# Kernel optimization log

Measured on AMD Instinct MI355X. Metric: run time of the kernel, lower is better.

The kernel has to match this reference:

```python
import math
import jax, jax.numpy as jnp
import numpy as np

INPUT_DIM = 1024
HEADS = 16
SEQ = 4096
BATCH = 1
SCALE = math.sqrt(INPUT_DIM / HEADS)  # 8.0


def setup_inputs() -> dict:
    key = jax.random.key(0)
    ks = jax.random.split(key, 5)
    D = INPUT_DIM
    return {
        "x": jax.random.normal(ks[0], (BATCH, SEQ, D), dtype=jnp.float32),
        "w_qkv": jax.random.normal(ks[1], (3 * D, D), dtype=jnp.float32) * (1.0 / math.sqrt(D)),
        "b_qkv": jax.random.normal(ks[2], (3 * D,), dtype=jnp.float32) * 0.01,
        "w_out": jax.random.normal(ks[3], (D, D), dtype=jnp.float32) * (1.0 / math.sqrt(D)),
        "b_out": jax.random.normal(ks[4], (D,), dtype=jnp.float32) * 0.01,
    }


def reference(x, w_qkv, b_qkv, w_out, b_out):
    b, n, D = x.shape
    h = HEADS
    d = D // h
    # qkv projection: [b, n, 3D]
    qkv = x @ w_qkv.T + b_qkv
    # 'b n (c h d) -> b c h n d' with c=3 outermost
    qkv = qkv.reshape(b, n, 3, h, d).transpose(2, 0, 3, 1, 4)  # [3, b, h, n, d]
    q, k, v = qkv[0], qkv[1], qkv[2]
    q = q / SCALE
    attn = jnp.einsum('bhnd,bhmd->bhnm', q, k)  # [b, h, n, n]
    attn = jax.nn.softmax(attn, axis=-1)
    # dropout is identity in eval mode
    context = jnp.einsum('bhnm,bhmd->bhnd', attn, v)  # [b, h, n, d]
    context = context.transpose(0, 2, 1, 3).reshape(b, n, D)  # 'b h n d -> b n (h d)'
    return context @ w_out.T + b_out
```

## Files before the change

### kernel.cpp

```cpp
#include <hip/hip_runtime.h>

typedef unsigned short u16;
typedef unsigned int u32;
typedef __attribute__((ext_vector_type(8))) short short8;
typedef __attribute__((ext_vector_type(4))) float f32x4;

__device__ __forceinline__ u16 f2b(float f) {
  union { float f; unsigned u; } v; v.f = f;
  unsigned r = (v.u + 0x7FFFu + ((v.u >> 16) & 1u)) >> 16;
  return (u16)r;
}
__device__ __forceinline__ float b2f(u16 b) {
  union { unsigned u; float f; } v; v.u = ((unsigned)b) << 16;
  return v.f;
}
__device__ __forceinline__ u32 cvtpk(float a, float b) {
  u32 r;
  asm("v_cvt_pk_bf16_f32 %0, %1, %2" : "=v"(r) : "v"(a), "v"(b));
  return r;
}
__device__ __forceinline__ void p32swap(u32& a, u32& b) {
  asm("v_permlane32_swap_b32 %0, %1" : "+v"(a), "+v"(b));
}
__device__ __forceinline__ void p16swap(u32& a, u32& b) {
  asm("v_permlane16_swap_b32 %0, %1" : "+v"(a), "+v"(b));
}
__device__ __forceinline__ float ldf(const void* p, size_t i, int f32) {
  return f32 ? ((const float*)p)[i] : b2f(((const u16*)p)[i]);
}

__global__ __launch_bounds__(256) void detect_dtype(const u16* __restrict__ x,
                                                    int* __restrict__ flag) {
  __shared__ int cnt;
  if (threadIdx.x == 0) cnt = 0;
  __syncthreads();
  int local = 0;
  for (int p = threadIdx.x; p < 512; p += 256) {
    int e = (x[2 * p] >> 7) & 0xFF;
    if (e >= 0xC0) local++;
  }
  atomicAdd(&cnt, local);
  __syncthreads();
  if (threadIdx.x == 0) flag[0] = (cnt >= 16) ? 1 : 0;
}

__global__ __launch_bounds__(256) void convert_all(
    const void* __restrict__ px, const void* __restrict__ pwq,
    const void* __restrict__ pbq, const void* __restrict__ pwo,
    const void* __restrict__ pbo, u16* __restrict__ xb,
    u16* __restrict__ wqkvb, u16* __restrict__ bqkvb, u16* __restrict__ wob,
    u16* __restrict__ bob) {
  __shared__ int sf;
  if (threadIdx.x == 0) sf = 0;
  __syncthreads();
  {
    const u16* xr = (const u16*)px;
    int local = 0;
    for (int p = threadIdx.x; p < 512; p += 256) {
      int e = (xr[2 * p] >> 7) & 0xFF;
      if (e >= 0xC0) local++;
    }
    atomicAdd(&sf, local);
  }
  __syncthreads();
  const int isf32 = (sf >= 16);

  int i = blockIdx.x * 256 + threadIdx.x;
  const void* in; u16* out; size_t g;
  if (i < 524288)       { in = px;  out = xb;    g = (size_t)i; }
  else if (i < 917504)  { in = pwq; out = wqkvb; g = (size_t)(i - 524288); }
  else if (i < 917888)  { in = pbq; out = bqkvb; g = (size_t)(i - 917504); }
  else if (i < 1048960) { in = pwo; out = wob;   g = (size_t)(i - 917888); }
  else                  { in = pbo; out = bob;   g = (size_t)(i - 1048960); }
  size_t base = g * 8;
  if (isf32) {
    const float* p = (const float*)in + base;
    float4 v0 = *(const float4*)p, v1 = *(const float4*)(p + 4);
    union { short8 v; u16 e[8]; } t;
    t.e[0]=f2b(v0.x); t.e[1]=f2b(v0.y); t.e[2]=f2b(v0.z); t.e[3]=f2b(v0.w);
    t.e[4]=f2b(v1.x); t.e[5]=f2b(v1.y); t.e[6]=f2b(v1.z); t.e[7]=f2b(v1.w);
    *(short8*)(out + base) = t.v;
  } else {
    *(short8*)(out + base) = *(const short8*)((const u16*)in + base);
  }
}

__global__ __launch_bounds__(256) void transpose_v(const u16* __restrict__ qkv,
                                                   u16* __restrict__ Vt) {
  __shared__ u16 T[64 * 72];
  const int tid = threadIdx.x;
  const int h = blockIdx.y;
  const int s0 = blockIdx.x * 64;
  for (int r = 0; r < 2; ++r) {
    int cid = r * 256 + tid;
    int s = cid >> 3, c8 = cid & 7;
    union { short8 v; u16 u[8]; } uu;
    uu.v = *(const short8*)(qkv + (size_t)(s0 + s) * 3072 + 2048 + h * 64 + c8 * 8);
    for (int i = 0; i < 8; ++i) T[(c8 * 8 + i) * 72 + s] = uu.u[i];
  }
  __syncthreads();
  for (int r = 0; r < 2; ++r) {
    int cid = r * 256 + tid;
    int dd = cid >> 3, c8 = cid & 7;
    union { short8 v; u16 u[8]; } uu;
    for (int i = 0; i < 8; ++i) uu.u[i] = T[dd * 72 + c8 * 8 + i];
    *(short8*)(Vt + (size_t)(h * 64 + dd) * 4096 + s0 + c8 * 8) = uu.v;
  }
}

__global__ __launch_bounds__(256) void gemm_bt(const void* __restrict__ A,
                                               const void* __restrict__ B,
                                               const void* __restrict__ bias,
                                               void* __restrict__ C,
                                               int M, int N, int K,
                                               int lda, int ldb, int ldc,
                                               int aMay, int bMay, int outF32,
                                               const int* __restrict__ flag) {
  __shared__ __align__(16) u16 sm[128 * 132];
  u16* As = sm;
  u16* Bs = sm + 128 * 64;
  const int f = flag[0];
  const int a32 = aMay && f, b32 = bMay && f;
  const int tid = threadIdx.x;
  const int w = tid >> 6, lane = tid & 63;
  const int lq = lane & 15, qr = lane >> 4;
  const int m0 = blockIdx.y * 128, n0 = blockIdx.x * 128;
  const int wm = (w >> 1) * 64, wn = (w & 1) * 64;

  f32x4 acc[4][4];
  for (int i = 0; i < 4; i++)
    for (int j = 0; j < 4; j++) acc[i][j] = (f32x4){0.f, 0.f, 0.f, 0.f};
  float bv[4];
  for (int ns = 0; ns < 4; ++ns) bv[ns] = ldf(bias, n0 + wn + ns * 16 + lq, b32);

  const int rs = tid >> 3, cs = tid & 7;
  const u16* gA = (const u16*)A + (size_t)(m0 + rs) * lda + cs * 8;
  const u16* gB = (const u16*)B + (size_t)(n0 + rs) * ldb + cs * 8;
  u16* lA = As + ((tid & ~63) << 3);
  u16* lB = Bs + ((tid & ~63) << 3);

  for (int k0 = 0; k0 < K; k0 += 64) {
    if (!(a32 | b32)) {
      for (int r = 0; r < 4; ++r) {
        __builtin_amdgcn_global_load_lds(gA + (size_t)(r * 32) * lda + k0,
                                         lA + r * 2048, 16, 0, 0);
        __builtin_amdgcn_global_load_lds(gB + (size_t)(r * 32) * ldb + k0,
                                         lB + r * 2048, 16, 0, 0);
      }
    } else {
      for (int r = 0; r < 4; ++r) {
        int cid = r * 256 + tid;
        int row = cid >> 3, c = cid & 7;
        if (a32) {
          const float* p = (const float*)A + (size_t)(m0 + row) * lda + k0 + c * 8;
          float4 v0 = *(const float4*)p, v1 = *(const float4*)(p + 4);
          union { short8 v; u16 e[8]; } t;
          t.e[0]=f2b(v0.x); t.e[1]=f2b(v0.y); t.e[2]=f2b(v0.z); t.e[3]=f2b(v0.w);
          t.e[4]=f2b(v1.x); t.e[5]=f2b(v1.y); t.e[6]=f2b(v1.z); t.e[7]=f2b(v1.w);
          *(short8*)(As + row * 64 + c * 8) = t.v;
        } else {
          *(short8*)(As + row * 64 + c * 8) =
              *(const short8*)((const u16*)A + (size_t)(m0 + row) * lda + k0 + c * 8);
        }
        if (b32) {
          const float* p = (const float*)B + (size_t)(n0 + row) * ldb + k0 + c * 8;
          float4 v0 = *(const float4*)p, v1 = *(const float4*)(p + 4);
          union { short8 v; u16 e[8]; } t;
          t.e[0]=f2b(v0.x); t.e[1]=f2b(v0.y); t.e[2]=f2b(v0.z); t.e[3]=f2b(v0.w);
          t.e[4]=f2b(v1.x); t.e[5]=f2b(v1.y); t.e[6]=f2b(v1.z); t.e[7]=f2b(v1.w);
          *(short8*)(Bs + row * 64 + c * 8) = t.v;
        } else {
          *(short8*)(Bs + row * 64 + c * 8) =
              *(const short8*)((const u16*)B + (size_t)(n0 + row) * ldb + k0 + c * 8);
        }
      }
    }
    __syncthreads();
    for (int ks = 0; ks < 2; ++ks) {
      short8 af[4], bf[4];
      const int sw = ks * 4 + qr;
      for (int i = 0; i < 4; i++) {
        af[i] = *(const short8*)(As + (wm + i * 16 + lq) * 64 + sw * 8);
        bf[i] = *(const short8*)(Bs + (wn + i * 16 + lq) * 64 + sw * 8);
      }
      for (int mi = 0; mi < 4; mi++)
        for (int ni = 0; ni < 4; ni++)
          acc[mi][ni] = __builtin_amdgcn_mfma_f32_16x16x32_bf16(
              af[mi], bf[ni], acc[mi][ni], 0, 0, 0);
    }
    __syncthreads();
  }

  if (!outF32) {
    u16* SH = sm;
    for (int mi = 0; mi < 4; mi++)
      for (int ni = 0; ni < 4; ni++)
        for (int r = 0; r < 4; ++r)
          SH[(wm + mi * 16 + qr * 4 + r) * 132 + wn + ni * 16 + lq] =
              f2b(acc[mi][ni][r] + bv[ni]);
    __syncthreads();
    for (int it = 0; it < 8; ++it) {
      int idx = it * 256 + tid;
      int row = idx >> 4, c8 = idx & 15;
      *(short8*)((u16*)C + (size_t)(m0 + row) * ldc + n0 + c8 * 8) =
          *(const short8*)(SH + row * 132 + c8 * 8);
    }
  } else {
    float* SHf = (float*)sm;
    for (int half = 0; half < 2; ++half) {
      if (half) __syncthreads();
      if ((w >> 1) == half) {
        for (int mi = 0; mi < 4; mi++)
          for (int ni = 0; ni < 4; ni++)
            for (int r = 0; r < 4; ++r)
              SHf[(mi * 16 + qr * 4 + r) * 132 + wn + ni * 16 + lq] =
                  acc[mi][ni][r] + bv[ni];
      }
      __syncthreads();
      for (int it = 0; it < 8; ++it) {
        int idx = it * 256 + tid;
        int row = idx >> 5, c4 = idx & 31;
        *(float4*)((float*)C + (size_t)(m0 + half * 64 + row) * ldc + n0 + c4 * 4) =
            *(const float4*)(SHf + row * 132 + c4 * 4);
      }
    }
  }
}

__global__ __launch_bounds__(512, 2) void attn_split(const u16* __restrict__ qkv,
                                                     const u16* __restrict__ Vtg,
                                                     u16* __restrict__ ctx, int ldctx) {
  __shared__ __align__(16) u16 SMEM[16384];
  const int tid = threadIdx.x;
  const int w = tid >> 6, lane = tid & 63;
  const int half = w >> 2, wq = w & 3;
  const int lq = lane & 15, qr = lane >> 4;
  const int qb = blockIdx.x, h = blockIdx.y;
  const int qbase = qb * 128 + wq * 32;
  const float cs = 0.18033688011112042f;

  u16* Kh = SMEM + half * 4096;
  u16* Vh = SMEM + 8192 + half * 4096;

  short8 qf[2][2];
#pragma unroll
  for (int mi = 0; mi < 2; ++mi)
#pragma unroll
    for (int ks = 0; ks < 2; ++ks)
      qf[mi][ks] = *(const short8*)(qkv + (size_t)(qbase + mi * 16 + lq) * 3072 +
                                    h * 64 + ks * 32 + qr * 8);

  f32x4 o[2][4];
#pragma unroll
  for (int mi = 0; mi < 2; ++mi)
#pragma unroll
    for (int ds = 0; ds < 4; ++ds) o[mi][ds] = (f32x4){0.f, 0.f, 0.f, 0.f};
  float lrow[2] = {0.f, 0.f};

  const int ht = tid & 255;
  const int c = ht & 7, r0 = ht >> 3;
  u16* dKA = Kh + r0 * 64 + ((c ^ (r0 & 7)) << 3);
  u16* dKB = dKA + 32 * 64;
  u16* dVA = Vh + r0 * 64 + ((c ^ (r0 & 7)) << 3);
  u16* dVB = dVA + 32 * 64;
  const u16* sKA = qkv + (size_t)(half * 2048 + r0) * 3072 + 1024 + h * 64 + c * 8;
  const u16* sKB = sKA + (size_t)32 * 3072;
  const u16* sVA = Vtg + (size_t)(h * 64 + r0) * 4096 + half * 2048 + c * 8;
  const u16* sVB = sVA + (size_t)32 * 4096;

  short8 rKA, rKB, rVA, rVB;
  rKA = *(const short8*)sKA; sKA += (size_t)64 * 3072;
  rKB = *(const short8*)sKB; sKB += (size_t)64 * 3072;
  rVA = *(const short8*)sVA; sVA += 64;
  rVB = *(const short8*)sVB; sVB += 64;

  for (int it = 0; it < 32; ++it) {
    __syncthreads();
    *(short8*)dKA = rKA;
    *(short8*)dKB = rKB;
    *(short8*)dVA = rVA;
    *(short8*)dVB = rVB;
    __syncthreads();

    if (it + 1 < 32) {
      rKA = *(const short8*)sKA; sKA += (size_t)64 * 3072;
      rKB = *(const short8*)sKB; sKB += (size_t)64 * 3072;
      rVA = *(const short8*)sVA; sVA += 64;
      rVB = *(const short8*)sVB; sVB += 64;
    }

    f32x4 s[2][4];
#pragma unroll
    for (int mi = 0; mi < 2; ++mi)
#pragma unroll
      for (int ns = 0; ns < 4; ++ns) s[mi][ns] = (f32x4){0.f, 0.f, 0.f, 0.f};
#pragma unroll
    for (int ks = 0; ks < 2; ++ks) {
      short8 kf[4];
#pragma unroll
      for (int ns = 0; ns < 4; ++ns) {
        int rk = ns * 16 + lq;
        kf[ns] = *(const short8*)(Kh + rk * 64 + (((ks * 4 + qr) ^ (lq & 7)) << 3));
      }
      __builtin_amdgcn_s_setprio(1);
#pragma unroll
      for (int mi = 0; mi < 2; ++mi)
#pragma unroll
        for (int ns = 0; ns < 4; ++ns)
          s[mi][ns] = __builtin_amdgcn_mfma_f32_16x16x32_bf16(
              kf[ns], qf[mi][ks], s[mi][ns], 0, 0, 0);
      __builtin_amdgcn_s_setprio(0);
    }

    short8 pf[2][2];
#pragma unroll
    for (int mi = 0; mi < 2; ++mi) {
      float lacc = 0.f;
      u32 X[4], Y[4];
#pragma unroll
      for (int ns = 0; ns < 4; ++ns) {
        float p0 = __builtin_amdgcn_exp2f(fmaf(s[mi][ns][0], cs, -12.0f));
        float p1 = __builtin_amdgcn_exp2f(fmaf(s[mi][ns][1], cs, -12.0f));
        float p2 = __builtin_amdgcn_exp2f(fmaf(s[mi][ns][2], cs, -12.0f));
        float p3 = __builtin_amdgcn_exp2f(fmaf(s[mi][ns][3], cs, -12.0f));
        lacc += (p0 + p1) + (p2 + p3);
        X[ns] = cvtpk(p0, p1);
        Y[ns] = cvtpk(p2, p3);
      }
      lrow[mi] += lacc;
#pragma unroll
      for (int ks = 0; ks < 2; ++ks) {
        u32 a0 = X[2 * ks], b0 = X[2 * ks + 1];
        u32 a1 = Y[2 * ks], b1 = Y[2 * ks + 1];
        p32swap(a0, b0); p16swap(a0, b0);
        p32swap(a1, b1); p16swap(a1, b1);
        union { u32 u[4]; short8 v; } t;
        t.u[0] = a0; t.u[1] = a1; t.u[2] = b0; t.u[3] = b1;
        pf[mi][ks] = t.v;
      }
    }

#pragma unroll
    for (int ks = 0; ks < 2; ++ks) {
      short8 vf[4];
#pragma unroll
      for (int ds = 0; ds < 4; ++ds) {
        int dv = ds * 16 + lq;
        vf[ds] = *(const short8*)(Vh + (size_t)dv * 64 +
                                  (((ks * 4 + qr) ^ (lq & 7)) << 3));
      }
      __builtin_amdgcn_s_setprio(1);
#pragma unroll
      for (int mi = 0; mi < 2; ++mi)
#pragma unroll
        for (int ds = 0; ds < 4; ++ds)
          o[mi][ds] = __builtin_amdgcn_mfma_f32_16x16x32_bf16(
              vf[ds], pf[mi][ks], o[mi][ds], 0, 0, 0);
      __builtin_amdgcn_s_setprio(0);
    }
  }

  __syncthreads();
  float* CB = (float*)SMEM;
#pragma unroll
  for (int mi = 0; mi < 2; ++mi) {
    float* p = CB + (size_t)(wq * 64 + lane) * 17;
    if (half == 1) {
#pragma unroll
      for (int ds = 0; ds < 4; ++ds) {
        p[ds * 4 + 0] = o[mi][ds][0];
        p[ds * 4 + 1] = o[mi][ds][1];
        p[ds * 4 + 2] = o[mi][ds][2];
        p[ds * 4 + 3] = o[mi][ds][3];
      }
      p[16] = lrow[mi];
    }
    __syncthreads();
    if (half == 0) {
#pragma unroll
      for (int ds = 0; ds < 4; ++ds) {
        o[mi][ds][0] += p[ds * 4 + 0];
        o[mi][ds][1] += p[ds * 4 + 1];
        o[mi][ds][2] += p[ds * 4 + 2];
        o[mi][ds][3] += p[ds * 4 + 3];
      }
      lrow[mi] += p[16];
    }
    __syncthreads();
  }

  if (half == 0) {
#pragma unroll
    for (int mi = 0; mi < 2; ++mi) {
      float l = lrow[mi];
      l += __shfl_xor(l, 16, 64);
      l += __shfl_xor(l, 32, 64);
      float linv = 1.f / fmaxf(l, 1e-30f);
      int row = qbase + mi * 16 + lq;
      u16* dst = ctx + (size_t)row * ldctx + h * 64 + qr * 4;
#pragma unroll
      for (int ds = 0; ds < 4; ++ds) {
        u32 lo = cvtpk(o[mi][ds][0] * linv, o[mi][ds][1] * linv);
        u32 hi = cvtpk(o[mi][ds][2] * linv, o[mi][ds][3] * linv);
        *(uint2*)(dst + ds * 16) = make_uint2(lo, hi);
      }
    }
  }
}

__global__ __launch_bounds__(256) void attn_fused(const u16* __restrict__ qkv,
                                                  const u16* __restrict__ Vtg,
                                                  u16* __restrict__ ctx, int ldctx) {
  __shared__ u16 Ks[64 * 64];
  __shared__ u16 Vts[64 * 64];
  const int tid = threadIdx.x;
  const int w = tid >> 6, lane = tid & 63;
  const int lq = lane & 15, qr = lane >> 4;
  const int qb = blockIdx.x, h = blockIdx.y;
  const int qbase = qb * 128 + w * 32;
  const float cs = 0.18033688011112042f;

  short8 qf[2][2];
  for (int mi = 0; mi < 2; ++mi)
    for (int ks = 0; ks < 2; ++ks)
      qf[mi][ks] = *(const short8*)(qkv + (size_t)(qbase + mi * 16 + lq) * 3072 +
                                    h * 64 + ks * 32 + qr * 8);

  f32x4 o[2][4];
  for (int mi = 0; mi < 2; ++mi)
    for (int ds = 0; ds < 4; ++ds) o[mi][ds] = (f32x4){0.f, 0.f, 0.f, 0.f};
  float lrow[2] = {0.f, 0.f};

  const int c = tid & 7, r0 = tid >> 3;
  u16* dKA = Ks + r0 * 64 + ((c ^ (r0 & 7)) << 3);
  u16* dKB = dKA + 32 * 64;
  u16* dVA = Vts + r0 * 64 + ((c ^ (r0 & 7)) << 3);
  u16* dVB = dVA + 32 * 64;
  const u16* sKA = qkv + (size_t)r0 * 3072 + 1024 + h * 64 + c * 8;
  const u16* sKB = sKA + (size_t)32 * 3072;
  const u16* sVA = Vtg ? (Vtg + (size_t)(h * 64 + r0) * 4096 + c * 8) : nullptr;
  const u16* sVB = Vtg ? (sVA + (size_t)32 * 4096) : nullptr;
  const u16* sVfA = qkv + (size_t)r0 * 3072 + 2048 + h * 64 + c * 8;
  const u16* sVfB = sVfA + (size_t)32 * 3072;

  short8 rKA, rKB, rVA, rVB;
  union { short8 v; u16 e[8]; } ufA, ufB;
  rKA = *(const short8*)sKA; sKA += (size_t)64 * 3072;
  rKB = *(const short8*)sKB; sKB += (size_t)64 * 3072;
  if (Vtg) {
    rVA = *(const short8*)sVA; sVA += 64;
    rVB = *(const short8*)sVB; sVB += 64;
  } else {
    ufA.v = *(const short8*)sVfA; sVfA += (size_t)64 * 3072;
    ufB.v = *(const short8*)sVfB; sVfB += (size_t)64 * 3072;
  }

  for (int j0 = 0; j0 < 4096; j0 += 64) {
    __syncthreads();
    *(short8*)dKA = rKA;
    *(short8*)dKB = rKB;
    if (Vtg) {
      *(short8*)dVA = rVA;
      *(short8*)dVB = rVB;
    } else {
      {
        const int jc = r0 >> 3;
        for (int i = 0; i < 8; ++i)
          Vts[(c * 8 + i) * 64 + ((jc ^ i) << 3) + (r0 & 7)] = ufA.e[i];
      }
      {
        const int jc = (r0 + 32) >> 3;
        for (int i = 0; i < 8; ++i)
          Vts[(c * 8 + i) * 64 + ((jc ^ i) << 3) + (r0 & 7)] = ufB.e[i];
      }
    }
    __syncthreads();

    if (j0 + 64 < 4096) {
      rKA = *(const short8*)sKA; sKA += (size_t)64 * 3072;
      rKB = *(const short8*)sKB; sKB += (size_t)64 * 3072;
      if (Vtg) {
        rVA = *(const short8*)sVA; sVA += 64;
        rVB = *(const short8*)sVB; sVB += 64;
      } else {
        ufA.v = *(const short8*)sVfA; sVfA += (size_t)64 * 3072;
        ufB.v = *(const short8*)sVfB; sVfB += (size_t)64 * 3072;
      }
    }

    f32x4 s[2][4];
    for (int mi = 0; mi < 2; ++mi)
      for (int ns = 0; ns < 4; ++ns) s[mi][ns] = (f32x4){0.f, 0.f, 0.f, 0.f};
    for (int ks = 0; ks < 2; ++ks) {
      short8 kf[4];
      for (int ns = 0; ns < 4; ++ns) {
        int rk = ns * 16 + lq;
        kf[ns] = *(const short8*)(Ks + rk * 64 + (((ks * 4 + qr) ^ (lq & 7)) << 3));
      }
      __builtin_amdgcn_s_setprio(1);
      for (int mi = 0; mi < 2; ++mi)
        for (int ns = 0; ns < 4; ++ns)
          s[mi][ns] = __builtin_amdgcn_mfma_f32_16x16x32_bf16(
              kf[ns], qf[mi][ks], s[mi][ns], 0, 0, 0);
      __builtin_amdgcn_s_setprio(0);
    }

    short8 pf[2][2];
#pragma unroll
    for (int mi = 0; mi < 2; ++mi) {
      float lacc = 0.f;
      u32 X[4], Y[4];
#pragma unroll
      for (int ns = 0; ns < 4; ++ns) {
        float p0 = __builtin_amdgcn_exp2f(fmaf(s[mi][ns][0], cs, -12.0f));
        float p1 = __builtin_amdgcn_exp2f(fmaf(s[mi][ns][1], cs, -12.0f));
        float p2 = __builtin_amdgcn_exp2f(fmaf(s[mi][ns][2], cs, -12.0f));
        float p3 = __builtin_amdgcn_exp2f(fmaf(s[mi][ns][3], cs, -12.0f));
        lacc += (p0 + p1) + (p2 + p3);
        X[ns] = cvtpk(p0, p1);
        Y[ns] = cvtpk(p2, p3);
      }
      lrow[mi] += lacc;
#pragma unroll
      for (int ks = 0; ks < 2; ++ks) {
        u32 a0 = X[2 * ks], b0 = X[2 * ks + 1];
        u32 a1 = Y[2 * ks], b1 = Y[2 * ks + 1];
        p32swap(a0, b0); p16swap(a0, b0);
        p32swap(a1, b1); p16swap(a1, b1);
        union { u32 u[4]; short8 v; } t;
        t.u[0] = a0; t.u[1] = a1; t.u[2] = b0; t.u[3] = b1;
        pf[mi][ks] = t.v;
      }
    }

    for (int ks = 0; ks < 2; ++ks) {
      short8 vf[4];
      for (int ds = 0; ds < 4; ++ds) {
        int dv = ds * 16 + lq;
        vf[ds] = *(const short8*)(Vts + (size_t)dv * 64 +
                                  (((ks * 4 + qr) ^ (lq & 7)) << 3));
      }
      __builtin_amdgcn_s_setprio(1);
      for (int mi = 0; mi < 2; ++mi)
        for (int ds = 0; ds < 4; ++ds)
          o[mi][ds] = __builtin_amdgcn_mfma_f32_16x16x32_bf16(
              vf[ds], pf[mi][ks], o[mi][ds], 0, 0, 0);
      __builtin_amdgcn_s_setprio(0);
    }
  }

  for (int mi = 0; mi < 2; ++mi) {
    float l = lrow[mi];
    l += __shfl_xor(l, 16, 64);
    l += __shfl_xor(l, 32, 64);
    float linv = 1.f / fmaxf(l, 1e-30f);
    int row = qbase + mi * 16 + lq;
    u16* dst = ctx + (size_t)row * ldctx + h * 64 + qr * 4;
    for (int ds = 0; ds < 4; ++ds) {
      u32 lo = cvtpk(o[mi][ds][0] * linv, o[mi][ds][1] * linv);
      u32 hi = cvtpk(o[mi][ds][2] * linv, o[mi][ds][3] * linv);
      *(uint2*)(dst + ds * 16) = make_uint2(lo, hi);
    }
  }
}

extern "C" void kernel_launch(void* const* d_in, const int* in_sizes, int n_in,
                              void* d_out, int out_size, void* d_ws, size_t ws_size,
                              hipStream_t stream) {
  float* out = (float*)d_out;

  const void *px = nullptr, *pwq = nullptr, *pbq = nullptr, *pwo = nullptr, *pbo = nullptr;
  if (n_in == 5) {
    for (int i = 0; i < 5; ++i) {
      switch (in_sizes[i]) {
        case 4194304: px = d_in[i]; break;
        case 3145728: pwq = d_in[i]; break;
        case 3072:    pbq = d_in[i]; break;
        case 1048576: pwo = d_in[i]; break;
        case 1024:    pbo = d_in[i]; break;
        default: break;
      }
    }
  }
  if (!px || !pwq || !pbq || !pwo || !pbo) {
    px = d_in[0]; pwq = d_in[1]; pbq = d_in[2]; pwo = d_in[3]; pbo = d_in[4];
  }

  int* flag = (int*)d_ws;
  u16* qkv = (u16*)((char*)d_ws + 64);
  u16* ctx = qkv;

  const size_t nQKV = (size_t)4096 * 3072;
  const size_t nVt = (size_t)16 * 64 * 4096;
  const size_t nx = 4194304, nwq = 3145728, nwo = 1048576;
  u16* Vtg = qkv + nQKV;
  const size_t need_vt = 64 + (nQKV + nVt) * 2;
  const size_t need_full = need_vt + (nx + nwq + 4096 + nwo + 1024) * 2;

  if (ws_size >= need_full) {
    u16* xb    = Vtg + nVt;
    u16* wqkvb = xb + nx;
    u16* bqkvb = wqkvb + nwq;
    u16* wob   = bqkvb + 4096;
    u16* bob   = wob + nwo;
    convert_all<<<4098, 256, 0, stream>>>(px, pwq, pbq, pwo, pbo,
                                          xb, wqkvb, bqkvb, wob, bob);

    gemm_bt<<<dim3(24, 32), 256, 0, stream>>>(xb, wqkvb, bqkvb, qkv,
                                              4096, 3072, 1024, 1024, 1024, 3072,
                                              0, 0, 0, flag);
    transpose_v<<<dim3(64, 16), 256, 0, stream>>>(qkv, Vtg);
    attn_split<<<dim3(32, 16), 512, 0, stream>>>(qkv, Vtg, ctx, 3072);
    gemm_bt<<<dim3(8, 32), 256, 0, stream>>>(ctx, wob, bob, out,
                                             4096, 1024, 1024, 3072, 1024, 1024,
                                             0, 0, 1, flag);
  } else if (ws_size >= need_vt) {
    detect_dtype<<<1, 256, 0, stream>>>((const u16*)px, flag);
    gemm_bt<<<dim3(24, 32), 256, 0, stream>>>(px, pwq, pbq, qkv,
                                              4096, 3072, 1024, 1024, 1024, 3072,
                                              1, 1, 0, flag);
    transpose_v<<<dim3(64, 16), 256, 0, stream>>>(qkv, Vtg);
    attn_split<<<dim3(32, 16), 512, 0, stream>>>(qkv, Vtg, ctx, 3072);
    gemm_bt<<<dim3(8, 32), 256, 0, stream>>>(ctx, pwo, pbo, out,
                                             4096, 1024, 1024, 3072, 1024, 1024,
                                             0, 1, 1, flag);
  } else {
    detect_dtype<<<1, 256, 0, stream>>>((const u16*)px, flag);
    gemm_bt<<<dim3(24, 32), 256, 0, stream>>>(px, pwq, pbq, qkv,
                                              4096, 3072, 1024, 1024, 1024, 3072,
                                              1, 1, 0, flag);
    attn_fused<<<dim3(32, 16), 256, 0, stream>>>(qkv, (const u16*)nullptr, ctx, 3072);
    gemm_bt<<<dim3(8, 32), 256, 0, stream>>>(ctx, pwo, pbo, out,
                                             4096, 1024, 1024, 3072, 1024, 1024,
                                             0, 1, 1, flag);
  }
}
```

Measured before the change: 272.5 us.

## Double-buffer attention K/V tiles via direct global-to-LDS loads

Replaces the register-staged K/V tile loads in the split attention kernel with `global_load_lds` direct-to-LDS transfers into a double-buffered shared-memory tile. The swizzle moves from the LDS store address to the global source column. The next tile is issued at the start of each iteration, and only one barrier per iteration remains instead of two. This is meant to overlap K/V fetch with the MFMA work and free the staging registers, at the cost of doubling LDS per block, which may pressure occupancy.

```diff
diff --git a/kernel.cpp b/kernel.cpp
--- a/kernel.cpp
+++ b/kernel.cpp
@@ -230,18 +230,15 @@
 __global__ __launch_bounds__(512, 2) void attn_split(const u16* __restrict__ qkv,
                                                      const u16* __restrict__ Vtg,
                                                      u16* __restrict__ ctx, int ldctx) {
-  __shared__ __align__(16) u16 SMEM[16384];
+  __shared__ __align__(16) u16 SMEM[2][16384];
   const int tid = threadIdx.x;
   const int w = tid >> 6, lane = tid & 63;
-  const int half = w >> 2, wq = w & 3;
+  const int half = w >> 2, wq = w & 3, wl = w & 3;
   const int lq = lane & 15, qr = lane >> 4;
   const int qb = blockIdx.x, h = blockIdx.y;
   const int qbase = qb * 128 + wq * 32;
   const float cs = 0.18033688011112042f;
 
-  u16* Kh = SMEM + half * 4096;
-  u16* Vh = SMEM + 8192 + half * 4096;
-
   short8 qf[2][2];
 #pragma unroll
   for (int mi = 0; mi < 2; ++mi)
@@ -257,37 +254,34 @@
     for (int ds = 0; ds < 4; ++ds) o[mi][ds] = (f32x4){0.f, 0.f, 0.f, 0.f};
   float lrow[2] = {0.f, 0.f};
 
-  const int ht = tid & 255;
-  const int c = ht & 7, r0 = ht >> 3;
-  u16* dKA = Kh + r0 * 64 + ((c ^ (r0 & 7)) << 3);
-  u16* dKB = dKA + 32 * 64;
-  u16* dVA = Vh + r0 * 64 + ((c ^ (r0 & 7)) << 3);
-  u16* dVB = dVA + 32 * 64;
-  const u16* sKA = qkv + (size_t)(half * 2048 + r0) * 3072 + 1024 + h * 64 + c * 8;
-  const u16* sKB = sKA + (size_t)32 * 3072;
-  const u16* sVA = Vtg + (size_t)(h * 64 + r0) * 4096 + half * 2048 + c * 8;
-  const u16* sVB = sVA + (size_t)32 * 4096;
-
-  short8 rKA, rKB, rVA, rVB;
-  rKA = *(const short8*)sKA; sKA += (size_t)64 * 3072;
-  rKB = *(const short8*)sKB; sKB += (size_t)64 * 3072;
-  rVA = *(const short8*)sVA; sVA += 64;
-  rVB = *(const short8*)sVB; sVB += 64;
+  const int csw = ((lane & 7) ^ (lane >> 3)) << 3;
+  const int r0v = wl * 8 + (lane >> 3);
+  const u16* sK0 = qkv + (size_t)(half * 2048 + r0v) * 3072 + 1024 + h * 64 + csw;
+  const u16* sK1 = sK0 + (size_t)32 * 3072;
+  const u16* sV0 = Vtg + (size_t)(h * 64 + r0v) * 4096 + half * 2048 + csw;
+  const u16* sV1 = sV0 + (size_t)32 * 4096;
+  const int kb = half * 4096 + wl * 512;
+  const int vb = 8192 + half * 4096 + wl * 512;
+
+#define STAGE(buf)                                                          \
+  do {                                                                      \
+    u16* B_ = &SMEM[buf][0];                                                \
+    __builtin_amdgcn_global_load_lds(sK0, B_ + kb, 16, 0, 0);               \
+    __builtin_amdgcn_global_load_lds(sK1, B_ + kb + 2048, 16, 0, 0);        \
+    __builtin_amdgcn_global_load_lds(sV0, B_ + vb, 16, 0, 0);               \
+    __builtin_amdgcn_global_load_lds(sV1, B_ + vb + 2048, 16, 0, 0);        \
+    sK0 += (size_t)64 * 3072; sK1 += (size_t)64 * 3072;                     \
+    sV0 += 64; sV1 += 64;                                                   \
+  } while (0)
+
+  STAGE(0);
+  __syncthreads();
 
   for (int it = 0; it < 32; ++it) {
-    __syncthreads();
-    *(short8*)dKA = rKA;
-    *(short8*)dKB = rKB;
-    *(short8*)dVA = rVA;
-    *(short8*)dVB = rVB;
-    __syncthreads();
-
-    if (it + 1 < 32) {
-      rKA = *(const short8*)sKA; sKA += (size_t)64 * 3072;
-      rKB = *(const short8*)sKB; sKB += (size_t)64 * 3072;
-      rVA = *(const short8*)sVA; sVA += 64;
-      rVB = *(const short8*)sVB; sVB += 64;
-    }
+    const int cur = it & 1;
+    if (it + 1 < 32) STAGE(cur ^ 1);
+    const u16* Kh = &SMEM[cur][half * 4096];
+    const u16* Vh = &SMEM[cur][8192 + half * 4096];
 
     f32x4 s[2][4];
 #pragma unroll
@@ -358,10 +352,11 @@
               vf[ds], pf[mi][ks], o[mi][ds], 0, 0, 0);
       __builtin_amdgcn_s_setprio(0);
     }
-  }
-
-  __syncthreads();
-  float* CB = (float*)SMEM;
+    __syncthreads();
+  }
+#undef STAGE
+
+  float* CB = (float*)&SMEM[0][0];
 #pragma unroll
   for (int mi = 0; mi < 2; ++mi) {
     float* p = CB + (size_t)(wq * 64 + lane) * 17;
```

After: 257.6 us. 1.06x faster.
